# Kernel optimization log

Measured on AMD Instinct MI355X. Metric: run time of the kernel, lower is better.

The kernel has to match this reference:

```python
import jax, jax.numpy as jnp
import numpy as np

B, T, D, H, P = 2, 2048, 1024, 16, 64  # batch, seq, d_model, heads, head_dim


def setup_inputs() -> dict:
    key = jax.random.key(0)
    ks = jax.random.split(key, 8)
    s = 0.02
    return {
        "Q": jax.random.normal(ks[0], (B, T, D), jnp.float32),
        "K": jax.random.normal(ks[1], (B, T, D), jnp.float32),
        "V": jax.random.normal(ks[2], (B, T, D), jnp.float32),
        "mask": jnp.ones((B, 1, 1, T), jnp.float32),
        "WQ": jax.random.normal(ks[3], (H, D, P), jnp.float32) * s,
        "WK": jax.random.normal(ks[4], (H, D, P), jnp.float32) * s,
        "WV": jax.random.normal(ks[5], (H, D, P), jnp.float32) * s,
        "rel_emb": jax.random.normal(ks[6], (2 * T - 1, P), jnp.float32) * s,
        "dense_W": jax.random.normal(ks[7], (H * P, D), jnp.float32) * s,
        "dense_b": jnp.zeros((D,), jnp.float32),
    }


def reference(Q, K, V, mask, WQ, WK, WV, rel_emb, dense_W, dense_b):
    # multi-head projections: (B,T,D) x (H,D,P) -> (B,H,T,P)
    q = jnp.einsum("btd,hdp->bhtp", Q, WQ)
    k = jnp.einsum("btd,hdp->bhtp", K, WK)
    v = jnp.einsum("btd,hdp->bhtp", V, WV)

    Tq = q.shape[2]
    # Shaw-style additive relative positional encoding from Q:
    # bias[b,h,i,j] = q[b,h,i] . rel_emb[j - i + T - 1]
    a = jnp.einsum("bhtp,rp->bhtr", q, rel_emb)          # (B,H,T,2T-1)
    rel_idx = jnp.arange(Tq)[None, :] - jnp.arange(Tq)[:, None] + (Tq - 1)  # (T,T)
    rpe = jnp.take_along_axis(a, rel_idx[None, None], axis=-1)              # (B,H,T,T)

    scale = 1.0 / jnp.sqrt(jnp.asarray(P, q.dtype))
    energies = (jnp.einsum("bhtp,bhsp->bhts", q, k) + rpe) * scale
    energies = energies + (1.0 - mask) * -1e9
    alphas = jax.nn.softmax(energies, axis=-1)
    ctx = jnp.einsum("bhts,bhsp->bhtp", alphas, v)        # (B,H,T,P)

    ctx = jnp.transpose(ctx, (0, 2, 1, 3)).reshape(ctx.shape[0], Tq, H * P)
    return ctx @ dense_W + dense_b
```

## Files before the change

### kernel.cpp

```cpp
#include <hip/hip_runtime.h>
#include <hip/hip_bf16.h>

typedef __bf16 bf16_t;
typedef __bf16 bf16x8 __attribute__((ext_vector_type(8)));
typedef float f32x4 __attribute__((ext_vector_type(4)));

#define QSCALE 0.1803368801111396f
#define MLOG2E 1.4426950408889634f

__device__ __forceinline__ f32x4 mfma16(bf16x8 a, bf16x8 b, f32x4 c) {
  return __builtin_amdgcn_mfma_f32_16x16x32_bf16(a, b, c, 0, 0, 0);
}

#define GLDS16(gsrc, ldst)                                                     \
  __builtin_amdgcn_global_load_lds(                                            \
      (const __attribute__((address_space(1))) void*)(gsrc),                   \
      (__attribute__((address_space(3))) void*)(ldst), 16, 0, 0)

__device__ __forceinline__ unsigned short bhalf(float f) {
  return __builtin_bit_cast(unsigned short, (bf16_t)f);
}

__global__ void prep_kernel(const float* __restrict__ rel,
                            const float* __restrict__ mask,
                            bf16_t* __restrict__ relb,
                            float* __restrict__ mbias) {
  int idx = blockIdx.x * 256 + threadIdx.x;
  if (idx < 4096 * 64) {
    int row = idx >> 6;
    int col = idx & 63;
    int sr = row > 4094 ? 4094 : row;
    relb[idx] = (bf16_t)rel[sr * 64 + col];
  } else {
    int j = idx - 4096 * 64;
    if (j < 4096) mbias[j] = (1.0f - mask[j]) * -1e9f * MLOG2E;
  }
}

__global__ __launch_bounds__(256) void proj_gemm_kernel(
    const float* __restrict__ Q, const float* __restrict__ K,
    const float* __restrict__ V, const float* __restrict__ WQ,
    const float* __restrict__ WK, const float* __restrict__ WV,
    bf16_t* __restrict__ qb, bf16_t* __restrict__ kb,
    bf16_t* __restrict__ vb) {
  const int z = blockIdx.z;
  const float* A = z == 0 ? Q : (z == 1 ? K : V);
  const float* W = z == 0 ? WQ : (z == 1 ? WK : WV);
  bf16_t* out = z == 0 ? qb : (z == 1 ? kb : vb);
  const float scale = z == 0 ? QSCALE : 1.0f;

  __shared__ bf16_t As[128][72];
  __shared__ bf16_t Bs[128][72];
  const int tid = threadIdx.x;
  const int lane = tid & 63;
  const int wid = tid >> 6;
  const int wm = wid >> 1, wn = wid & 1;
  const int row0 = blockIdx.x * 128;
  const int col0 = blockIdx.y * 128;
  const int lr = lane & 15;
  const int lk = (lane >> 4) * 8;

  f32x4 acc[4][4];
#pragma unroll
  for (int m = 0; m < 4; m++)
#pragma unroll
    for (int n = 0; n < 4; n++) acc[m][n] = {0.f, 0.f, 0.f, 0.f};

  for (int kt = 0; kt < 1024; kt += 64) {
#pragma unroll
    for (int i = 0; i < 4; i++) {
      int c = tid + i * 256;
      int row = c >> 3;
      int k8 = (c & 7) * 8;
      const float* src = A + (size_t)(row0 + row) * 1024 + kt + k8;
      bf16_t* dst = &As[row][k8];
#pragma unroll
      for (int j = 0; j < 8; j++) dst[j] = (bf16_t)src[j];
    }
#pragma unroll
    for (int i = 0; i < 4; i++) {
      int c = tid + i * 256;
      int col = c & 127;
      int k8 = (c >> 7) * 8;
      int gcol = col0 + col;
      int h = gcol >> 6, p = gcol & 63;
      const float* src = W + (size_t)h * 65536 + (size_t)(kt + k8) * 64 + p;
      bf16_t* dst = &Bs[col][k8];
#pragma unroll
      for (int j = 0; j < 8; j++) dst[j] = (bf16_t)src[j * 64];
    }
    __syncthreads();
#pragma unroll
    for (int kk = 0; kk < 2; kk++) {
      bf16x8 af[4], bfr[4];
#pragma unroll
      for (int m = 0; m < 4; m++)
        af[m] = *(const bf16x8*)&As[wm * 64 + m * 16 + lr][kk * 32 + lk];
#pragma unroll
      for (int n = 0; n < 4; n++)
        bfr[n] = *(const bf16x8*)&Bs[wn * 64 + n * 16 + lr][kk * 32 + lk];
#pragma unroll
      for (int m = 0; m < 4; m++)
#pragma unroll
        for (int n = 0; n < 4; n++)
          acc[m][n] = mfma16(af[m], bfr[n], acc[m][n]);
    }
    __syncthreads();
  }
  const int rb = (lane >> 4) * 4;
#pragma unroll
  for (int m = 0; m < 4; m++) {
#pragma unroll
    for (int n = 0; n < 4; n++) {
      int col = col0 + wn * 64 + n * 16 + lr;
      int h = col >> 6, p = col & 63;
      int row_base = row0 + wm * 64 + m * 16 + rb;
      int b = row_base >> 11, t0 = row_base & 2047;
      if (z == 2) {
        unsigned u0 = ((unsigned)bhalf(acc[m][n][1]) << 16) | bhalf(acc[m][n][0]);
        unsigned u1 = ((unsigned)bhalf(acc[m][n][3]) << 16) | bhalf(acc[m][n][2]);
        uint2 u = {u0, u1};
        *(uint2*)&out[(((size_t)(b * 16 + h) * 64 + p) * 2048) + t0] = u;
      } else {
#pragma unroll
        for (int r = 0; r < 4; r++) {
          out[(((size_t)(b * 16 + h) * 2048 + t0 + r) * 64) + p] =
              (bf16_t)(acc[m][n][r] * scale);
        }
      }
    }
  }
}

__global__ __launch_bounds__(256) void dense_gemm_kernel(
    const bf16_t* __restrict__ A, const float* __restrict__ W,
    const float* __restrict__ bias, float* __restrict__ out) {
  __shared__ bf16_t As[128][72];
  __shared__ bf16_t Bs[128][72];
  const int tid = threadIdx.x;
  const int lane = tid & 63;
  const int wid = tid >> 6;
  const int wm = wid >> 1, wn = wid & 1;
  const int row0 = blockIdx.x * 128;
  const int col0 = blockIdx.y * 128;
  const int lr = lane & 15;
  const int lk = (lane >> 4) * 8;

  f32x4 acc[4][4];
#pragma unroll
  for (int m = 0; m < 4; m++)
#pragma unroll
    for (int n = 0; n < 4; n++) acc[m][n] = {0.f, 0.f, 0.f, 0.f};

  for (int kt = 0; kt < 1024; kt += 64) {
#pragma unroll
    for (int i = 0; i < 4; i++) {
      int c = tid + i * 256;
      int row = c >> 3;
      int k8 = (c & 7) * 8;
      *(uint4*)&As[row][k8] =
          *(const uint4*)(A + (size_t)(row0 + row) * 1024 + kt + k8);
    }
#pragma unroll
    for (int i = 0; i < 4; i++) {
      int c = tid + i * 256;
      int col = c & 127;
      int k8 = (c >> 7) * 8;
      const float* src = W + (size_t)(kt + k8) * 1024 + col0 + col;
      bf16_t* dst = &Bs[col][k8];
#pragma unroll
      for (int j = 0; j < 8; j++) dst[j] = (bf16_t)src[j * 1024];
    }
    __syncthreads();
#pragma unroll
    for (int kk = 0; kk < 2; kk++) {
      bf16x8 af[4], bfr[4];
#pragma unroll
      for (int m = 0; m < 4; m++)
        af[m] = *(const bf16x8*)&As[wm * 64 + m * 16 + lr][kk * 32 + lk];
#pragma unroll
      for (int n = 0; n < 4; n++)
        bfr[n] = *(const bf16x8*)&Bs[wn * 64 + n * 16 + lr][kk * 32 + lk];
#pragma unroll
      for (int m = 0; m < 4; m++)
#pragma unroll
        for (int n = 0; n < 4; n++)
          acc[m][n] = mfma16(af[m], bfr[n], acc[m][n]);
    }
    __syncthreads();
  }
  const int rb = (lane >> 4) * 4;
#pragma unroll
  for (int m = 0; m < 4; m++) {
#pragma unroll
    for (int n = 0; n < 4; n++) {
      int col = col0 + wn * 64 + n * 16 + lr;
      float bv = bias[col];
#pragma unroll
      for (int r = 0; r < 4; r++) {
        int row = row0 + wm * 64 + m * 16 + rb + r;
        out[(size_t)row * 1024 + col] = acc[m][n][r] + bv;
      }
    }
  }
}

__global__ __launch_bounds__(256, 2) void attn_kernel(
    const bf16_t* __restrict__ qg, const bf16_t* __restrict__ kg,
    const bf16_t* __restrict__ vt, const bf16_t* __restrict__ relb,
    const float* __restrict__ mbias, bf16_t* __restrict__ ctx) {
  __shared__ bf16_t Kb[2][64 * 64];
  __shared__ bf16_t Vb[64 * 64];
  __shared__ bf16_t Rr[4][64 * 64];
  __shared__ unsigned EL[4][16 * 41];
  __shared__ bf16_t PL[4][16 * 72];

  const int tid = threadIdx.x;
  const int lane = tid & 63;
  const int w = tid >> 6;

  const int id = blockIdx.x;
  const int id2 = (id & 7) * 64 + (id >> 3);
  const int it = id2 & 15;
  const int bh = id2 >> 4;
  const int h = bh & 15;
  const int b = bh >> 4;
  const int i0 = it * 128;

  const size_t base = ((size_t)bh) * 2048 * 64;
  const int lr = lane & 15;
  const int g = lane >> 4;
  const int lk = g * 8;
  const int srow = lane >> 3;
  const int t16 = lane & 7;
  const int swz = (lr & 7) << 3;

  const bf16_t* kgb = kg + base;
  const bf16_t* vgb = vt + base;
  const bf16_t* rgb = relb + (size_t)(1920 - i0) * 64;

  bf16x8 aq[2][2];
#pragma unroll
  for (int gq = 0; gq < 2; gq++) {
    const bf16_t* src =
        qg + base + (size_t)(i0 + w * 32 + gq * 16 + lr) * 64 + lk;
    aq[gq][0] = *(const bf16x8*)(src);
    aq[gq][1] = *(const bf16x8*)(src + 32);
  }

  float m0 = -INFINITY, l0 = 0.f, m1 = -INFINITY, l1 = 0.f;
  f32x4 o0[4], o1[4];
#pragma unroll
  for (int n = 0; n < 4; n++) {
    o0[n] = {0.f, 0.f, 0.f, 0.f};
    o1[n] = {0.f, 0.f, 0.f, 0.f};
  }

  const float* mb_base = mbias + (size_t)b * 2048;

#pragma unroll
  for (int i = 0; i < 2; i++) {
    int chunk = i * 4 + w;
    int row = chunk * 8 + srow;
    GLDS16(kgb + row * 64 + ((t16 ^ (row & 7)) * 8),
           Kb[0] + chunk * 512 + lane * 8);
  }
#pragma unroll
  for (int c = 0; c < 3; c++) {
#pragma unroll
    for (int i = 0; i < 2; i++) {
      int chunk = i * 4 + w;
      int row = chunk * 8 + srow;
      GLDS16(rgb + (size_t)(c * 64 + row) * 64 + ((t16 ^ (row & 7)) * 8),
             Rr[c] + chunk * 512 + lane * 8);
    }
  }
  __syncthreads();

  for (int jt = 0; jt < 32; jt++) {
    const int j0 = jt * 64;

#pragma unroll
    for (int i = 0; i < 2; i++) {
      int chunk = i * 4 + w;
      int p = chunk * 8 + srow;
      GLDS16(vgb + j0 + (size_t)p * 2048 + ((t16 ^ (p & 7)) * 8),
             Vb + chunk * 512 + lane * 8);
    }
    if (jt < 31) {
      const bf16_t* kn = kgb + (size_t)(j0 + 64) * 64;
      bf16_t* kd = Kb[(jt + 1) & 1];
#pragma unroll
      for (int i = 0; i < 2; i++) {
        int chunk = i * 4 + w;
        int row = chunk * 8 + srow;
        GLDS16(kn + row * 64 + ((t16 ^ (row & 7)) * 8),
               kd + chunk * 512 + lane * 8);
      }
      const bf16_t* rs = rgb + (size_t)(jt + 3) * 64 * 64;
      bf16_t* rd = Rr[(jt + 3) & 3];
#pragma unroll
      for (int i = 0; i < 2; i++) {
        int chunk = i * 4 + w;
        int row = chunk * 8 + srow;
        GLDS16(rs + row * 64 + ((t16 ^ (row & 7)) * 8),
               rd + chunk * 512 + lane * 8);
      }
    }

    f32x4 sacc0[4], sacc1[4], er0[5], er1[5];
#pragma unroll
    for (int n = 0; n < 4; n++) {
      sacc0[n] = {0.f, 0.f, 0.f, 0.f};
      sacc1[n] = {0.f, 0.f, 0.f, 0.f};
    }
#pragma unroll
    for (int n = 0; n < 5; n++) {
      er0[n] = {0.f, 0.f, 0.f, 0.f};
      er1[n] = {0.f, 0.f, 0.f, 0.f};
    }
    const bf16_t* kcur = Kb[jt & 1];
    __builtin_amdgcn_s_setprio(1);
#pragma unroll
    for (int kk = 0; kk < 2; kk++) {
      int cbs = (kk * 32 + lk) ^ swz;
#pragma unroll
      for (int n = 0; n < 4; n++) {
        bf16x8 ak = *(const bf16x8*)&kcur[(n * 16 + lr) * 64 + cbs];
        sacc0[n] = mfma16(ak, aq[0][kk], sacc0[n]);
        sacc1[n] = mfma16(ak, aq[1][kk], sacc1[n]);
      }
#pragma unroll
      for (int fi = 0; fi < 6; fi++) {
        int f = 6 - 2 * w + fi;
        const bf16_t* rc = Rr[(jt + (f >> 2)) & 3];
        bf16x8 ar = *(const bf16x8*)&rc[((f & 3) * 16 + lr) * 64 + cbs];
        if (fi >= 1) er0[fi - 1] = mfma16(ar, aq[0][kk], er0[fi - 1]);
        if (fi <= 4) er1[fi] = mfma16(ar, aq[1][kk], er1[fi]);
      }
    }
    __builtin_amdgcn_s_setprio(0);

    bf16x8 bp0[2], bp1[2];
#pragma unroll
    for (int gq = 0; gq < 2; gq++) {
      f32x4* sacc = gq ? sacc1 : sacc0;
      f32x4* er = gq ? er1 : er0;
      float m = gq ? m1 : m0;
      float l = gq ? l1 : l0;
      f32x4* o = gq ? o1 : o0;
#pragma unroll
      for (int n2 = 0; n2 < 5; n2++) {
        EL[w][lr * 41 + n2 * 8 + g * 2 + 0] =
            ((unsigned)bhalf(er[n2][1]) << 16) | bhalf(er[n2][0]);
        EL[w][lr * 41 + n2 * 8 + g * 2 + 1] =
            ((unsigned)bhalf(er[n2][3]) << 16) | bhalf(er[n2][2]);
      }
      float s[4][4];
#pragma unroll
      for (int n = 0; n < 4; n++) {
        f32x4 mbv = *(const f32x4*)&mb_base[j0 + n * 16 + g * 4];
#pragma unroll
        for (int r = 0; r < 4; r++) {
          int key = n * 16 + g * 4 + r;
          int idx = key - lr + 15;
          unsigned d = EL[w][lr * 41 + (idx >> 1)];
          float bias = __builtin_bit_cast(float, (d >> ((idx & 1) << 4)) << 16);
          s[n][r] = sacc[n][r] + bias + mbv[r];
        }
      }
      float a0 = fmaxf(fmaxf(s[0][0], s[0][1]), fmaxf(s[0][2], s[0][3]));
      float a1 = fmaxf(fmaxf(s[1][0], s[1][1]), fmaxf(s[1][2], s[1][3]));
      float a2 = fmaxf(fmaxf(s[2][0], s[2][1]), fmaxf(s[2][2], s[2][3]));
      float a3 = fmaxf(fmaxf(s[3][0], s[3][1]), fmaxf(s[3][2], s[3][3]));
      float pmx = fmaxf(fmaxf(a0, a1), fmaxf(a2, a3));
      pmx = fmaxf(pmx, __shfl_xor(pmx, 16, 64));
      pmx = fmaxf(pmx, __shfl_xor(pmx, 32, 64));
      if (!__all(pmx - m <= 8.f)) {
        float mnew = fmaxf(m, pmx);
        float fac = exp2f(m - mnew);
        m = mnew;
        l *= fac;
#pragma unroll
        for (int n = 0; n < 4; n++) {
          o[n][0] *= fac; o[n][1] *= fac; o[n][2] *= fac; o[n][3] *= fac;
        }
      }
      float ps = 0.f;
#pragma unroll
      for (int n = 0; n < 4; n++) {
        float e0 = exp2f(s[n][0] - m);
        float e1 = exp2f(s[n][1] - m);
        float e2 = exp2f(s[n][2] - m);
        float e3 = exp2f(s[n][3] - m);
        s[n][0] = e0; s[n][1] = e1; s[n][2] = e2; s[n][3] = e3;
        ps += (e0 + e1) + (e2 + e3);
      }
      ps += __shfl_xor(ps, 16, 64);
      ps += __shfl_xor(ps, 32, 64);
      l += ps;
      if (gq) { m1 = m; l1 = l; } else { m0 = m; l0 = l; }
#pragma unroll
      for (int n = 0; n < 4; n++) {
        unsigned u0 = ((unsigned)bhalf(s[n][1]) << 16) | bhalf(s[n][0]);
        unsigned u1 = ((unsigned)bhalf(s[n][3]) << 16) | bhalf(s[n][2]);
        uint2 u = {u0, u1};
        *(uint2*)&PL[w][lr * 72 + n * 16 + g * 4] = u;
      }
      if (gq) {
        bp1[0] = *(const bf16x8*)&PL[w][lr * 72 + lk];
        bp1[1] = *(const bf16x8*)&PL[w][lr * 72 + 32 + lk];
      } else {
        bp0[0] = *(const bf16x8*)&PL[w][lr * 72 + lk];
        bp0[1] = *(const bf16x8*)&PL[w][lr * 72 + 32 + lk];
      }
    }

    __syncthreads();

    __builtin_amdgcn_s_setprio(1);
#pragma unroll
    for (int kk = 0; kk < 2; kk++) {
      int cbs = (kk * 32 + lk) ^ swz;
#pragma unroll
      for (int n = 0; n < 4; n++) {
        bf16x8 av = *(const bf16x8*)&Vb[(n * 16 + lr) * 64 + cbs];
        o0[n] = mfma16(av, bp0[kk], o0[n]);
        o1[n] = mfma16(av, bp1[kk], o1[n]);
      }
    }
    __builtin_amdgcn_s_setprio(0);

    __syncthreads();
  }

#pragma unroll
  for (int gq = 0; gq < 2; gq++) {
    f32x4* o = gq ? o1 : o0;
    float inv = 1.0f / (gq ? l1 : l0);
    size_t bt = (size_t)b * 2048 + i0 + w * 32 + gq * 16 + lr;
#pragma unroll
    for (int n = 0; n < 4; n++) {
      unsigned u0 = ((unsigned)bhalf(o[n][1] * inv) << 16) | bhalf(o[n][0] * inv);
      unsigned u1 = ((unsigned)bhalf(o[n][3] * inv) << 16) | bhalf(o[n][2] * inv);
      uint2 u = {u0, u1};
      *(uint2*)&ctx[bt * 1024 + h * 64 + n * 16 + g * 4] = u;
    }
  }
}

extern "C" void kernel_launch(void* const* d_in, const int* in_sizes, int n_in,
                              void* d_out, int out_size, void* d_ws,
                              size_t ws_size, hipStream_t stream) {
  (void)in_sizes; (void)n_in; (void)out_size; (void)ws_size;
  const float* Q    = (const float*)d_in[0];
  const float* K    = (const float*)d_in[1];
  const float* V    = (const float*)d_in[2];
  const float* mask = (const float*)d_in[3];
  const float* WQ   = (const float*)d_in[4];
  const float* WK   = (const float*)d_in[5];
  const float* WV   = (const float*)d_in[6];
  const float* rel  = (const float*)d_in[7];
  const float* dW   = (const float*)d_in[8];
  const float* db   = (const float*)d_in[9];
  float* out = (float*)d_out;

  const size_t NQKV = (size_t)2 * 16 * 2048 * 64;
  bf16_t* qb   = (bf16_t*)d_ws;
  bf16_t* kb   = qb + NQKV;
  bf16_t* vb   = kb + NQKV;
  bf16_t* ctxb = vb + NQKV;
  bf16_t* relb = ctxb + NQKV;
  float*  mbias = (float*)(relb + 4096 * 64);

  dim3 blk(256);
  prep_kernel<<<dim3((4096 * 64 + 4096) / 256), blk, 0, stream>>>(rel, mask,
                                                                  relb, mbias);
  proj_gemm_kernel<<<dim3(32, 8, 3), blk, 0, stream>>>(Q, K, V, WQ, WK, WV, qb,
                                                       kb, vb);
  attn_kernel<<<dim3(512), blk, 0, stream>>>(qb, kb, vb, relb, mbias, ctxb);
  dense_gemm_kernel<<<dim3(32, 8), blk, 0, stream>>>(ctxb, dW, db, out);
}
```

Baseline: 216.1 us.

## Double-buffer V tiles and drop mid-iteration barrier in attention loop

After: 218.6 us. Within noise of the previous version (+1.1%).

```diff
diff --git a/kernel.cpp b/kernel.cpp
--- a/kernel.cpp
+++ b/kernel.cpp
@@ -210,10 +210,9 @@
     const bf16_t* __restrict__ vt, const bf16_t* __restrict__ relb,
     const float* __restrict__ mbias, bf16_t* __restrict__ ctx) {
   __shared__ bf16_t Kb[2][64 * 64];
-  __shared__ bf16_t Vb[64 * 64];
+  __shared__ bf16_t Vb[2][64 * 64];
   __shared__ bf16_t Rr[4][64 * 64];
-  __shared__ unsigned EL[4][16 * 41];
-  __shared__ bf16_t PL[4][16 * 72];
+  __shared__ unsigned SC[4][688];
 
   const int tid = threadIdx.x;
   const int lane = tid & 63;
@@ -257,6 +256,7 @@
   }
 
   const float* mb_base = mbias + (size_t)b * 2048;
+  unsigned* scw = SC[w];
 
 #pragma unroll
   for (int i = 0; i < 2; i++) {
@@ -266,6 +266,13 @@
            Kb[0] + chunk * 512 + lane * 8);
   }
 #pragma unroll
+  for (int i = 0; i < 2; i++) {
+    int chunk = i * 4 + w;
+    int p = chunk * 8 + srow;
+    GLDS16(vgb + (size_t)p * 2048 + ((t16 ^ (p & 7)) * 8),
+           Vb[0] + chunk * 512 + lane * 8);
+  }
+#pragma unroll
   for (int c = 0; c < 3; c++) {
 #pragma unroll
     for (int i = 0; i < 2; i++) {
@@ -280,14 +287,19 @@
   for (int jt = 0; jt < 32; jt++) {
     const int j0 = jt * 64;
 
-#pragma unroll
-    for (int i = 0; i < 2; i++) {
-      int chunk = i * 4 + w;
-      int p = chunk * 8 + srow;
-      GLDS16(vgb + j0 + (size_t)p * 2048 + ((t16 ^ (p & 7)) * 8),
-             Vb + chunk * 512 + lane * 8);
-    }
+    f32x4 mbv[4];
+#pragma unroll
+    for (int n = 0; n < 4; n++)
+      mbv[n] = *(const f32x4*)&mb_base[j0 + n * 16 + g * 4];
+
     if (jt < 31) {
+#pragma unroll
+      for (int i = 0; i < 2; i++) {
+        int chunk = i * 4 + w;
+        int p = chunk * 8 + srow;
+        GLDS16(vgb + (j0 + 64) + (size_t)p * 2048 + ((t16 ^ (p & 7)) * 8),
+               Vb[(jt + 1) & 1] + chunk * 512 + lane * 8);
+      }
       const bf16_t* kn = kgb + (size_t)(j0 + 64) * 64;
       bf16_t* kd = Kb[(jt + 1) & 1];
 #pragma unroll
@@ -351,22 +363,21 @@
       f32x4* o = gq ? o1 : o0;
 #pragma unroll
       for (int n2 = 0; n2 < 5; n2++) {
-        EL[w][lr * 41 + n2 * 8 + g * 2 + 0] =
-            ((unsigned)bhalf(er[n2][1]) << 16) | bhalf(er[n2][0]);
-        EL[w][lr * 41 + n2 * 8 + g * 2 + 1] =
-            ((unsigned)bhalf(er[n2][3]) << 16) | bhalf(er[n2][2]);
+        unsigned u0 = ((unsigned)bhalf(er[n2][1]) << 16) | bhalf(er[n2][0]);
+        unsigned u1 = ((unsigned)bhalf(er[n2][3]) << 16) | bhalf(er[n2][2]);
+        uint2 u = {u0, u1};
+        *(uint2*)&scw[lr * 42 + n2 * 8 + g * 2] = u;
       }
       float s[4][4];
 #pragma unroll
       for (int n = 0; n < 4; n++) {
-        f32x4 mbv = *(const f32x4*)&mb_base[j0 + n * 16 + g * 4];
 #pragma unroll
         for (int r = 0; r < 4; r++) {
           int key = n * 16 + g * 4 + r;
           int idx = key - lr + 15;
-          unsigned d = EL[w][lr * 41 + (idx >> 1)];
+          unsigned d = scw[lr * 42 + (idx >> 1)];
           float bias = __builtin_bit_cast(float, (d >> ((idx & 1) << 4)) << 16);
-          s[n][r] = sacc[n][r] + bias + mbv[r];
+          s[n][r] = sacc[n][r] + bias + mbv[n][r];
         }
       }
       float a0 = fmaxf(fmaxf(s[0][0], s[0][1]), fmaxf(s[0][2], s[0][3]));
@@ -405,26 +416,27 @@
         unsigned u0 = ((unsigned)bhalf(s[n][1]) << 16) | bhalf(s[n][0]);
         unsigned u1 = ((unsigned)bhalf(s[n][3]) << 16) | bhalf(s[n][2]);
         uint2 u = {u0, u1};
-        *(uint2*)&PL[w][lr * 72 + n * 16 + g * 4] = u;
-      }
+        *(uint2*)&scw[lr * 36 + n * 8 + g * 2] = u;
+      }
+      uint4 t0 = *(const uint4*)&scw[lr * 36 + g * 4];
+      uint4 t1 = *(const uint4*)&scw[lr * 36 + 16 + g * 4];
       if (gq) {
-        bp1[0] = *(const bf16x8*)&PL[w][lr * 72 + lk];
-        bp1[1] = *(const bf16x8*)&PL[w][lr * 72 + 32 + lk];
+        bp1[0] = __builtin_bit_cast(bf16x8, t0);
+        bp1[1] = __builtin_bit_cast(bf16x8, t1);
       } else {
-        bp0[0] = *(const bf16x8*)&PL[w][lr * 72 + lk];
-        bp0[1] = *(const bf16x8*)&PL[w][lr * 72 + 32 + lk];
-      }
-    }
-
-    __syncthreads();
-
+        bp0[0] = __builtin_bit_cast(bf16x8, t0);
+        bp0[1] = __builtin_bit_cast(bf16x8, t1);
+      }
+    }
+
+    const bf16_t* vcur = Vb[jt & 1];
     __builtin_amdgcn_s_setprio(1);
 #pragma unroll
     for (int kk = 0; kk < 2; kk++) {
       int cbs = (kk * 32 + lk) ^ swz;
 #pragma unroll
       for (int n = 0; n < 4; n++) {
-        bf16x8 av = *(const bf16x8*)&Vb[(n * 16 + lr) * 64 + cbs];
+        bf16x8 av = *(const bf16x8*)&vcur[(n * 16 + lr) * 64 + cbs];
         o0[n] = mfma16(av, bp0[kk], o0[n]);
         o1[n] = mfma16(av, bp1[kk], o1[n]);
       }
```
